# Kernel optimization log

Measured on AMD Instinct MI355X. Metric: run time of the kernel, lower is better.

The kernel has to match this reference:

```python
import jax, jax.numpy as jnp
import numpy as np
import math

TPE_DIM = 16
NEG_INF = -1e9


def temporal_positional_encoding(t, dim=TPE_DIM):
    # t: (B, S) continuous positions -> (B, S, dim) sinusoidal encoding
    half = dim // 2
    div_term = jnp.exp(jnp.arange(half, dtype=t.dtype) * (-math.log(10000.0) / dim) * 2.0)
    ang = t[..., None] * div_term  # (B, S, half)
    # interleave sin/cos: pe[..., 0::2]=sin, pe[..., 1::2]=cos
    pe = jnp.stack([jnp.sin(ang), jnp.cos(ang)], axis=-1)  # (B, S, half, 2)
    return pe.reshape(t.shape[0], t.shape[1], dim)


def setup_inputs() -> dict:
    key = jax.random.key(0)
    k1, k2, k3, k4 = jax.random.split(key, 4)
    B, P, S, D = 8, 32, 512, 64
    t = jax.random.uniform(k1, (B, S), dtype=jnp.float32)
    x = jax.random.normal(k2, (B, P, S, D), dtype=jnp.float32)
    mask = jax.random.randint(k3, (B, P, S), 0, 2).astype(jnp.float32)
    # nn.Linear(1,1) weight (only the weight is used in forward)
    alpha_w = jax.random.normal(k4, (1, 1), dtype=jnp.float32) * 0.1
    return {"t": t, "x": x, "mask": mask, "alpha_w": alpha_w}


def reference(t, x, mask, alpha_w):
    B, P, S, D = x.shape
    dk = jnp.float32(TPE_DIM)
    # max-min normalize t over the time dim
    t_min = jnp.min(t, axis=1, keepdims=True)
    t_max = jnp.max(t, axis=1, keepdims=True)
    tn = (t - t_min) / (t_max - t_min)
    # scale by (elu(alpha*1000, 1) + 1)
    scale = jax.nn.elu(alpha_w[0, 0] * 1000.0) + 1.0
    tn = scale * tn
    tpe = temporal_positional_encoding(tn)  # (B, S, TPE_DIM)
    # attention scores over time: (B, S, S), shared across p
    scores = jnp.einsum('bsd,btd->bst', tpe, tpe) / jnp.sqrt(dk)
    eye = jnp.eye(S, dtype=mask.dtype)
    # cond True where (mask_broadcast + eye) < 0.5 -> fill with -1e9
    cond = (mask[:, :, None, :] + eye[None, None, :, :]) < 0.5  # (B, P, S, S)
    sc = jnp.where(cond, jnp.float32(NEG_INF), scores[:, None, :, :])
    p_attn = jax.nn.softmax(sc, axis=-1)  # (B, P, S, S)
    inter_x = jnp.einsum('bpst,bptd->bpsd', p_attn, x)  # (B, P, S, D)
    m = mask[..., None]  # (B, P, S, 1)
    return x * m + inter_x * (1.0 - m)
```

## Files before the change

kernel.cpp:

```cpp
#include <hip/hip_runtime.h>
#include <math.h>

#define B_ 8
#define P_ 32
#define S_ 512
#define D_ 64

typedef __attribute__((ext_vector_type(4))) _Float16 half4;
typedef __attribute__((ext_vector_type(4))) float f32x4;

__launch_bounds__(512, 2)
__global__ void k_fused(const float* __restrict__ t, const float* __restrict__ alpha_w,
                        const float* __restrict__ x, const float* __restrict__ mask,
                        float* __restrict__ out) {
    const int bp = blockIdx.x & (B_ * P_ - 1);
    const int h  = blockIdx.x >> 8;
    const int b = bp >> 5;
    const int tid = threadIdx.x, lane = tid & 63, wave = tid >> 6;
    const int quad = lane >> 4, nl = lane & 15;

    __shared__ float maskL[S_];
    __shared__ short qidxL[S_];
    __shared__ int cntS;
    __shared__ float red[16];
    __shared__ __align__(16) _Float16 tpeP[S_][24];
    __shared__ __align__(16) _Float16 Xfrag[2][4][5][64][4];

    const float* maskBP = mask + (size_t)bp * S_;
    const float* xBP = x + (size_t)bp * S_ * D_;
    float* outBP = out + (size_t)bp * S_ * D_;

    float tv = t[b * S_ + tid];
    maskL[tid] = maskBP[tid];
    {
        float mn = tv, mx = tv;
#pragma unroll
        for (int o = 32; o > 0; o >>= 1) {
            mn = fminf(mn, __shfl_xor(mn, o, 64));
            mx = fmaxf(mx, __shfl_xor(mx, o, 64));
        }
        if (lane == 0) { red[wave] = mn; red[8 + wave] = mx; }
    }
    __syncthreads();
    float mn = red[0], mx = red[8];
#pragma unroll
    for (int w = 1; w < 8; w++) { mn = fminf(mn, red[w]); mx = fmaxf(mx, red[8 + w]); }

    float aw = alpha_w[0] * 1000.0f;
    float el = aw > 0.0f ? aw : (__expf(aw) - 1.0f);
    float inv = (el + 1.0f) / (mx - mn);

    {
        const float divs[8] = {1.0f, 0.31622776601683794f, 0.1f, 0.031622776601683791f,
                               0.01f, 0.0031622776601683794f, 0.001f, 0.00031622776601683794f};
        float tn = (tv - mn) * inv;
        half4 w[4];
#pragma unroll
        for (int f = 0; f < 8; f++) {
            float ang = tn * divs[f];
            w[f >> 1][(f & 1) * 2]     = (_Float16)(0.5f * __sinf(ang));
            w[f >> 1][(f & 1) * 2 + 1] = (_Float16)(0.5f * __cosf(ang));
        }
#pragma unroll
        for (int g = 0; g < 4; g++) *(half4*)&tpeP[tid][g * 4] = w[g];
    }

    if (wave == 0) {
        int nq = 0;
        for (int c = 0; c < 8; c++) {
            int tt = c * 64 + lane;
            bool isq = maskL[tt] < 0.5f;
            unsigned long long bm = __ballot(isq);
            int pb = __popcll(bm & ((1ull << lane) - 1ull));
            if (isq) qidxL[nq + pb] = (short)tt;
            nq += __popcll(bm);
        }
        if (lane == 0) cntS = nq;
    }
    __syncthreads();
    const int NQ = cntS;

    bool act[2];
    half4 bQ[2];
#pragma unroll
    for (int i = 0; i < 2; i++) {
        int qt = 2 * (wave + 8 * i) + h;
        act[i] = (qt * 16) < NQ;
        int rq = act[i] ? min(qt * 16 + nl, NQ - 1) : 0;
        int row = ((int)qidxL[rq]) & (S_ - 1);
        bQ[i] = *(const half4*)&tpeP[row][quad * 4];
    }

    f32x4 acc[2][5];
#pragma unroll
    for (int i = 0; i < 2; i++)
#pragma unroll
        for (int ct = 0; ct < 5; ct++) acc[i][ct] = (f32x4){0.f, 0.f, 0.f, 0.f};

    auto issue = [&](int kb, float v[2][4]) {
#pragma unroll
        for (int it = 0; it < 2; it++) {
            int item = it * 512 + tid;
            int d = item & 63, qd = (item >> 6) & 3, kt = (item >> 8) & 3;
            int key = kb + kt * 16 + qd * 4;
            const float* base = xBP + (size_t)key * D_ + d;
#pragma unroll
            for (int j = 0; j < 4; j++) v[it][j] = base[j * D_];
        }
    };
    auto commit = [&](int buf, int kb, float v[2][4]) {
#pragma unroll
        for (int it = 0; it < 2; it++) {
            int item = it * 512 + tid;
            int d = item & 63, qd = (item >> 6) & 3, kt = (item >> 8) & 3;
            int key = kb + kt * 16 + qd * 4;
            half4 w;
#pragma unroll
            for (int j = 0; j < 4; j++) {
                float mv = maskL[key + j];
                if (it == h && mv >= 0.5f)
                    outBP[(size_t)(key + j) * D_ + d] = v[it][j];
                w[j] = (_Float16)(v[it][j] * mv);
            }
            *(half4*)&Xfrag[buf][kt][d >> 4][qd * 16 + (d & 15)][0] = w;
        }
        if (tid < 256) {
            int kt = tid >> 6, l = tid & 63;
            int qd = l >> 4, m = l & 15;
            half4 w;
#pragma unroll
            for (int j = 0; j < 4; j++)
                w[j] = (m == 0) ? (_Float16)maskL[kb + kt * 16 + qd * 4 + j] : (_Float16)0.f;
            *(half4*)&Xfrag[buf][kt][4][l][0] = w;
        }
    };

    float v0[2][4];
    issue(0, v0);
    commit(0, 0, v0);
    __syncthreads();

    for (int c = 0; c < 8; c++) {
        float vn[2][4];
        if (c < 7) issue((c + 1) * 64, vn);

        const int buf = c & 1, kb = c * 64;
#pragma unroll
        for (int kt = 0; kt < 4; kt++) {
            half4 aK = *(const half4*)&tpeP[kb + kt * 16 + nl][quad * 4];
            half4 xA[5];
#pragma unroll
            for (int ct = 0; ct < 5; ct++)
                xA[ct] = *(const half4*)&Xfrag[buf][kt][ct][lane][0];
#pragma unroll
            for (int i = 0; i < 2; i++) {
                if (act[i]) {
                    f32x4 sT = __builtin_amdgcn_mfma_f32_16x16x16f16(
                        aK, bQ[i], (f32x4){0.f, 0.f, 0.f, 0.f}, 0, 0, 0);
                    half4 pt;
#pragma unroll
                    for (int j = 0; j < 4; j++) pt[j] = (_Float16)__expf(sT[j] - 2.0f);
#pragma unroll
                    for (int ct = 0; ct < 5; ct++)
                        acc[i][ct] = __builtin_amdgcn_mfma_f32_16x16x16f16(
                            xA[ct], pt, acc[i][ct], 0, 0, 0);
                }
            }
        }

        if (c < 7) commit(buf ^ 1, (c + 1) * 64, vn);
        __syncthreads();
    }

#pragma unroll
    for (int i = 0; i < 2; i++) {
        if (!act[i]) continue;
        int qt = 2 * (wave + 8 * i) + h;
        float den = __shfl(acc[i][4][0], nl, 64);
        float invd = 1.0f / (den + 1.0f);
        int rowl = qt * 16 + nl;
        if (rowl < NQ) {
            int sg = qidxL[rowl];
#pragma unroll
            for (int ct = 0; ct < 4; ct++) {
                const float4 xv = *(const float4*)(xBP + (size_t)sg * D_ + ct * 16 + quad * 4);
                float4 o;
                o.x = (acc[i][ct][0] + xv.x) * invd;
                o.y = (acc[i][ct][1] + xv.y) * invd;
                o.z = (acc[i][ct][2] + xv.z) * invd;
                o.w = (acc[i][ct][3] + xv.w) * invd;
                *(float4*)(outBP + (size_t)sg * D_ + ct * 16 + quad * 4) = o;
            }
        }
    }
}

extern "C" void kernel_launch(void* const* d_in, const int* in_sizes, int n_in,
                              void* d_out, int out_size, void* d_ws, size_t ws_size,
                              hipStream_t stream) {
    const float* t       = (const float*)d_in[0];
    const float* x       = (const float*)d_in[1];
    const float* mask    = (const float*)d_in[2];
    const float* alpha_w = (const float*)d_in[3];
    float* out = (float*)d_out;

    k_fused<<<dim3(B_ * P_ * 2), dim3(512), 0, stream>>>(t, alpha_w, x, mask, out);
}
```

Measured before the change: 104.4 us.

## Compact unmasked keys into index list and loop only over valid key chunks

Builds a compacted list of key positions whose mask is set, and iterates the key loop only over chunks of that list instead of all 512 positions. About half the keys are masked, so the streaming x loads and MFMA work shrink by roughly half. The mask multiply becomes a validity check on the padded tail. The cost is gathered, indirect row loads of x that coalesce less well. Launch bounds are also raised to ask for four blocks per CU, which squeezes registers and may cause spills.

```diff
diff --git a/kernel.cpp b/kernel.cpp
--- a/kernel.cpp
+++ b/kernel.cpp
@@ -9,7 +9,7 @@
 typedef __attribute__((ext_vector_type(4))) _Float16 half4;
 typedef __attribute__((ext_vector_type(4))) float f32x4;
 
-__launch_bounds__(512, 2)
+__launch_bounds__(512, 4)
 __global__ void k_fused(const float* __restrict__ t, const float* __restrict__ alpha_w,
                         const float* __restrict__ x, const float* __restrict__ mask,
                         float* __restrict__ out) {
@@ -21,7 +21,8 @@
 
     __shared__ float maskL[S_];
     __shared__ short qidxL[S_];
-    __shared__ int cntS;
+    __shared__ short kidxL[S_];
+    __shared__ int cntS[2];
     __shared__ float red[16];
     __shared__ __align__(16) _Float16 tpeP[S_][24];
     __shared__ __align__(16) _Float16 Xfrag[2][4][5][64][4];
@@ -66,19 +67,24 @@
     }
 
     if (wave == 0) {
-        int nq = 0;
+        int nq = 0, nk = 0;
         for (int c = 0; c < 8; c++) {
             int tt = c * 64 + lane;
             bool isq = maskL[tt] < 0.5f;
             unsigned long long bm = __ballot(isq);
             int pb = __popcll(bm & ((1ull << lane) - 1ull));
             if (isq) qidxL[nq + pb] = (short)tt;
-            nq += __popcll(bm);
-        }
-        if (lane == 0) cntS = nq;
+            else     kidxL[nk + (lane - pb)] = (short)tt;
+            int nqc = __popcll(bm);
+            nq += nqc;
+            nk += 64 - nqc;
+        }
+        if (lane == 0) { cntS[0] = nq; cntS[1] = nk; }
     }
     __syncthreads();
-    const int NQ = cntS;
+    const int NQ = cntS[0];
+    const int NK = cntS[1];
+    const int NCH = (NK + 63) >> 6;
 
     bool act[2];
     half4 bQ[2];
@@ -102,10 +108,12 @@
         for (int it = 0; it < 2; it++) {
             int item = it * 512 + tid;
             int d = item & 63, qd = (item >> 6) & 3, kt = (item >> 8) & 3;
-            int key = kb + kt * 16 + qd * 4;
-            const float* base = xBP + (size_t)key * D_ + d;
-#pragma unroll
-            for (int j = 0; j < 4; j++) v[it][j] = base[j * D_];
+            int ki = kb + kt * 16 + qd * 4;
+#pragma unroll
+            for (int j = 0; j < 4; j++) {
+                int key = (int)kidxL[min(ki + j, NK - 1)];
+                v[it][j] = xBP[(size_t)key * D_ + d];
+            }
         }
     };
     auto commit = [&](int buf, int kb, float v[2][4]) {
@@ -113,14 +121,14 @@
         for (int it = 0; it < 2; it++) {
             int item = it * 512 + tid;
             int d = item & 63, qd = (item >> 6) & 3, kt = (item >> 8) & 3;
-            int key = kb + kt * 16 + qd * 4;
+            int ki = kb + kt * 16 + qd * 4;
             half4 w;
 #pragma unroll
             for (int j = 0; j < 4; j++) {
-                float mv = maskL[key + j];
-                if (it == h && mv >= 0.5f)
-                    outBP[(size_t)(key + j) * D_ + d] = v[it][j];
-                w[j] = (_Float16)(v[it][j] * mv);
+                bool val = (ki + j) < NK;
+                if (it == h && val)
+                    outBP[(size_t)((int)kidxL[ki + j]) * D_ + d] = v[it][j];
+                w[j] = val ? (_Float16)v[it][j] : (_Float16)0.f;
             }
             *(half4*)&Xfrag[buf][kt][d >> 4][qd * 16 + (d & 15)][0] = w;
         }
@@ -130,24 +138,25 @@
             half4 w;
 #pragma unroll
             for (int j = 0; j < 4; j++)
-                w[j] = (m == 0) ? (_Float16)maskL[kb + kt * 16 + qd * 4 + j] : (_Float16)0.f;
+                w[j] = (m == 0 && (kb + kt * 16 + qd * 4 + j) < NK) ? (_Float16)1.f
+                                                                    : (_Float16)0.f;
             *(half4*)&Xfrag[buf][kt][4][l][0] = w;
         }
     };
 
     float v0[2][4];
-    issue(0, v0);
-    commit(0, 0, v0);
+    if (NCH > 0) { issue(0, v0); commit(0, 0, v0); }
     __syncthreads();
 
-    for (int c = 0; c < 8; c++) {
+    for (int c = 0; c < NCH; c++) {
         float vn[2][4];
-        if (c < 7) issue((c + 1) * 64, vn);
+        if (c + 1 < NCH) issue((c + 1) * 64, vn);
 
         const int buf = c & 1, kb = c * 64;
 #pragma unroll
         for (int kt = 0; kt < 4; kt++) {
-            half4 aK = *(const half4*)&tpeP[kb + kt * 16 + nl][quad * 4];
+            int krow = (int)kidxL[min(kb + kt * 16 + nl, NK - 1)];
+            half4 aK = *(const half4*)&tpeP[krow][quad * 4];
             half4 xA[5];
 #pragma unroll
             for (int ct = 0; ct < 5; ct++)
@@ -168,7 +177,7 @@
             }
         }
 
-        if (c < 7) commit(buf ^ 1, (c + 1) * 64, vn);
+        if (c + 1 < NCH) commit(buf ^ 1, (c + 1) * 64, vn);
         __syncthreads();
     }
 
```

After: 101.4 us. -2.8%, faster.
